# Kernel tuning notes

Hardware: AMD Instinct MI355X
Metric: run time of the kernel (lower is better)

Reference implementation:

```python
import jax, jax.numpy as jnp
import numpy as np

B = 131072
D_IN = 385          # 384-d embedding + 1 correctness feature
D_H = 192           # both trunk layers resolve to max(.,192)=192 per source
Q = 1000            # number of questions
C = 16              # classes per head (uniform padding of per-question heads)


def setup_inputs() -> dict:
    key = jax.random.key(0)
    ks = jax.random.split(key, 9)
    x = jax.random.normal(ks[0], (B, D_IN), dtype=jnp.float32)
    question_ids = jax.random.randint(ks[1], (B,), 0, Q, dtype=jnp.int32)
    is_correct = jax.random.randint(ks[2], (B,), 0, 2, dtype=jnp.int32)
    W1 = jax.random.normal(ks[3], (D_IN, D_H), dtype=jnp.float32) * 0.05
    b1 = jnp.zeros((D_H,), dtype=jnp.float32)
    W2 = jax.random.normal(ks[4], (D_H, D_H), dtype=jnp.float32) * 0.05
    b2 = jnp.zeros((D_H,), dtype=jnp.float32)
    # Head bank: slots [0,Q) = false heads, [Q,2Q) = true heads.
    W_heads = jax.random.normal(ks[5], (2 * Q, C, D_H), dtype=jnp.float32) * 0.05
    b_heads = jax.random.normal(ks[6], (2 * Q, C), dtype=jnp.float32) * 0.05
    return {"x": x, "question_ids": question_ids, "is_correct": is_correct,
            "W1": W1, "b1": b1, "W2": W2, "b2": b2,
            "W_heads": W_heads, "b_heads": b_heads}


def reference(x, question_ids, is_correct, W1, b1, W2, b2, W_heads, b_heads):
    # Shared trunk (eval mode: dropout = identity)
    h = jax.nn.relu(x @ W1 + b1)            # [B, 192]
    feat = jax.nn.relu(h @ W2 + b2)         # [B, 192]
    # Hard routing: pick true or false head for this question.
    Qn = W_heads.shape[0] // 2
    idx = question_ids + is_correct * Qn    # [B]
    Wq = W_heads[idx]                       # [B, C, 192] gather (memory-bound)
    bq = b_heads[idx]                       # [B, C]
    logits = jnp.einsum('bcd,bd->bc', Wq, feat) + bq  # per-sample routed linear
    return logits
```

## Files before the change

### kernel.cpp

```cpp
#include <hip/hip_runtime.h>
#include <hip/hip_bf16.h>
#include <stdint.h>
#include <stddef.h>


typedef short s8v __attribute__((ext_vector_type(8)));
typedef float f4v __attribute__((ext_vector_type(4)));
typedef float f4a __attribute__((ext_vector_type(4), aligned(4)));

typedef const void __attribute__((address_space(1))) *gas1_t;
typedef void __attribute__((address_space(3))) *las3_t;

namespace {
constexpr int kDin = 385;
constexpr int kDh  = 192;
constexpr int kQ   = 1000;
constexpr int kC   = 16;
constexpr int BM   = 64;
constexpr int BM2  = 128;
constexpr int NT   = 512;
constexpr int NK1  = 13;
constexpr int NK2  = 6;
constexpr int CHUNK = 12 * 64 * 8;
constexpr int H2   = 200;

constexpr size_t WS_W1   = 0;
constexpr size_t WS_W2   = 163840;
constexpr size_t WS_HIST = 245760;
constexpr size_t WS_CUR  = 253952;
constexpr size_t WS_PERM = 262144;

constexpr size_t WB_FEAT = 0;
constexpr size_t WB_W1   = 50331648;
constexpr size_t WB_W2   = WB_W1 + 159744;
constexpr size_t WB_HIST = WB_W2 + 73728;
constexpr size_t WB_CUR  = WB_HIST + 8192;
constexpr size_t WB_PERM = WB_CUR + 8192;
constexpr size_t WB_NEED = WB_PERM + 524288;
constexpr size_t WS_SANE_MAX = (1ull << 36);
}

__device__ __forceinline__ unsigned short f2bf(float f) {
  unsigned int u = __float_as_uint(f);
  u = u + 0x7fffu + ((u >> 16) & 1u);
  return (unsigned short)(u >> 16);
}

__device__ __forceinline__ unsigned int pk2(float lo, float hi) {
  union { __hip_bfloat162 h2; unsigned int u; } cv;
  cv.h2 = __float22bfloat162_rn(make_float2(lo, hi));
  return cv.u;
}

union s8u { s8v s; unsigned int u[4]; };

__device__ __forceinline__ void swz_one(const float* W, int K, int i,
                                        unsigned short* out) {
  int k = i / kDh;
  int c = i - k * kDh;
  float v = (k < K) ? W[(size_t)k * kDh + c] : 0.f;
  int oi = (k >> 5) * CHUNK + (((c >> 4) * 64 + ((k >> 3) & 3) * 16 + (c & 15)) << 3)
         + (k & 7);
  out[oi] = f2bf(v);
}

__global__ void combo_prep(const int* __restrict__ qid, const int* __restrict__ isc,
                           int B, int nbH,
                           const float* __restrict__ W1, const float* __restrict__ W2,
                           int* __restrict__ hist,
                           unsigned short* __restrict__ W1sw,
                           unsigned short* __restrict__ W2sw) {
  int bid = blockIdx.x;
  if (bid < nbH) {
    int i = bid * 256 + threadIdx.x;
    if (i < B) atomicAdd(&hist[qid[i] + isc[i] * kQ], 1);
  } else if (bid < nbH + 312) {
    swz_one(W1, kDin, (bid - nbH) * 256 + threadIdx.x, W1sw);
  } else {
    swz_one(W2, kDh, (bid - nbH - 312) * 256 + threadIdx.x, W2sw);
  }
}

__global__ __launch_bounds__(256)
void scatter2(const int* __restrict__ qid, const int* __restrict__ isc, int B,
              const int* __restrict__ hist, int* __restrict__ rank_ctr,
              int* __restrict__ perm) {
  __shared__ int sh[2048];
  __shared__ int ssum[256];
  int t = threadIdx.x;
  int4 a = ((const int4*)hist)[t * 2];
  int4 b = ((const int4*)hist)[t * 2 + 1];
  int s1 = a.x + a.y, s2 = s1 + a.z, s3 = s2 + a.w;
  int s4 = s3 + b.x, s5 = s4 + b.y, s6 = s5 + b.z, s7 = s6 + b.w;
  ssum[t] = s7;
  __syncthreads();
  #pragma unroll
  for (int d = 1; d < 256; d <<= 1) {
    int xv = (t >= d) ? ssum[t - d] : 0;
    __syncthreads();
    ssum[t] += xv;
    __syncthreads();
  }
  int base = ssum[t] - s7;
  sh[t * 8 + 0] = base;
  sh[t * 8 + 1] = base + a.x;
  sh[t * 8 + 2] = base + s1;
  sh[t * 8 + 3] = base + s2;
  sh[t * 8 + 4] = base + s3;
  sh[t * 8 + 5] = base + s4;
  sh[t * 8 + 6] = base + s5;
  sh[t * 8 + 7] = base + s6;
  __syncthreads();
  int i = blockIdx.x * 256 + t;
  if (i < B) {
    int h = qid[i] + isc[i] * kQ;
    int pos = sh[h] + atomicAdd(&rank_ctr[h], 1);
    perm[pos] = i;
  }
}

__device__ __forceinline__ void stage2(const unsigned short* gsrc,
                                       unsigned short* lbase, int tid) {
  const char* g = (const char*)gsrc + (size_t)tid * 16;
  char* l = (char*)lbase + ((tid >> 6) << 10);
  __builtin_amdgcn_global_load_lds((gas1_t)g, (las3_t)l, 16, 0, 0);
  if (tid < 256)
    __builtin_amdgcn_global_load_lds((gas1_t)(g + 8192), (las3_t)(l + 8192),
                                     16, 0, 0);
}

__global__ __launch_bounds__(NT, 4)
void trunk_k2(const float* __restrict__ x,
              const float* __restrict__ b1,
              const float* __restrict__ b2,
              const unsigned short* __restrict__ W1sw,
              const unsigned short* __restrict__ W2sw,
              unsigned short* __restrict__ featG) {
  __shared__ __align__(16) unsigned short hS[BM2 * H2];
  __shared__ __align__(16) unsigned short bS[2 * CHUNK];

  const int tid  = threadIdx.x;
  const int lane = tid & 63, wid = tid >> 6;
  const int m = lane & 15, quad = lane >> 4;
  const int w16 = wid * 16;
  const int row0 = blockIdx.x * BM2;

  const float* px = x + (size_t)(row0 + w16 + m) * kDin;

  stage2(W1sw, bS, tid);
  f4a c0 = *(const f4a*)(px + quad * 8);
  f4a c1 = *(const f4a*)(px + quad * 8 + 4);
  float tl = 0.f;

  f4v acc[12];
  #pragma unroll
  for (int t = 0; t < 12; ++t) acc[t] = (f4v){0.f, 0.f, 0.f, 0.f};
  __syncthreads();

  #pragma unroll
  for (int g = 0; g < NK1; ++g) {
    const unsigned short* np = (g < NK1 - 1)
        ? W1sw + (size_t)(g + 1) * CHUNK : W2sw;
    stage2(np, bS + ((g + 1) & 1) * CHUNK, tid);

    f4a n0, n1;
    if (g < NK1 - 2) {
      n0 = *(const f4a*)(px + (g + 1) * 32 + quad * 8);
      n1 = *(const f4a*)(px + (g + 1) * 32 + quad * 8 + 4);
    } else if (g == NK1 - 2) {
      tl = (quad == 0) ? px[384] : 0.f;
    }

    s8v a;
    if (g < NK1 - 1) {
      s8u ua;
      ua.u[0] = pk2(c0[0], c0[1]); ua.u[1] = pk2(c0[2], c0[3]);
      ua.u[2] = pk2(c1[0], c1[1]); ua.u[3] = pk2(c1[2], c1[3]);
      a = ua.s;
    } else {
      a = (s8v){0,0,0,0,0,0,0,0};
      a[0] = (short)f2bf(tl);
    }

    const unsigned short* bB = bS + (g & 1) * CHUNK;
    #pragma unroll
    for (int t = 0; t < 12; ++t) {
      s8v b = *(const s8v*)&bB[(t * 64 + lane) * 8];
      acc[t] = __builtin_amdgcn_mfma_f32_16x16x32_bf16(a, b, acc[t], 0, 0, 0);
    }

    if (g == NK1 - 1) {
      #pragma unroll
      for (int t = 0; t < 12; ++t) {
        int c = t * 16 + m;
        float bb = b1[c];
        #pragma unroll
        for (int r4 = 0; r4 < 4; ++r4) {
          int r = w16 + quad * 4 + r4;
          float v0 = acc[t][r4] + bb;
          hS[r * H2 + c] = f2bf(v0 > 0.f ? v0 : 0.f);
          acc[t][r4] = 0.f;
        }
      }
    }
    __syncthreads();
    if (g < NK1 - 2) { c0 = n0; c1 = n1; }
  }

  #pragma unroll
  for (int k2 = 0; k2 < NK2; ++k2) {
    const int g = NK1 + k2;
    if (k2 < NK2 - 1)
      stage2(W2sw + (size_t)(k2 + 1) * CHUNK,
             bS + ((g + 1) & 1) * CHUNK, tid);

    s8v a = *(const s8v*)&hS[(w16 + m) * H2 + k2 * 32 + quad * 8];
    const unsigned short* bB = bS + (g & 1) * CHUNK;
    #pragma unroll
    for (int t = 0; t < 12; ++t) {
      s8v b = *(const s8v*)&bB[(t * 64 + lane) * 8];
      acc[t] = __builtin_amdgcn_mfma_f32_16x16x32_bf16(a, b, acc[t], 0, 0, 0);
    }
    if (k2 < NK2 - 1) __syncthreads();
  }

  #pragma unroll
  for (int t = 0; t < 12; ++t) {
    int c = t * 16 + m;
    float bb = b2[c];
    #pragma unroll
    for (int r4 = 0; r4 < 4; ++r4) {
      int r = w16 + quad * 4 + r4;
      float v0 = acc[t][r4] + bb;
      hS[r * H2 + c] = f2bf(v0 > 0.f ? v0 : 0.f);
    }
  }
  __syncthreads();

  #pragma unroll
  for (int j = 0; j < 6; ++j) {
    int e = tid + j * NT;
    int row = e / 24, c8 = e - row * 24;
    *(s8v*)&featG[(size_t)(row0 + row) * kDh + c8 * 8] =
        *(const s8v*)&hS[row * H2 + c8 * 8];
  }
}

__global__ __launch_bounds__(NT, 8)
void head_k(const int* __restrict__ qid, const int* __restrict__ isc,
            const float* __restrict__ Wh, const float* __restrict__ bh,
            const unsigned short* __restrict__ featG,
            const int* __restrict__ perm, float* __restrict__ out) {
  __shared__ int permS[BM];
  __shared__ int idxS[BM];

  const int tid  = threadIdx.x;
  const int lane = tid & 63, wid = tid >> 6;
  const int m = lane & 15, quad = lane >> 4;
  const int rh = wid >> 1, ch = wid & 1;
  const int row0 = blockIdx.x * BM;

  if (tid < BM) {
    int p = perm[row0 + tid];
    permS[tid] = p;
    idxS[tid] = qid[p] + isc[p] * kQ;
  }
  __syncthreads();

  const int w16 = rh * 16;
  const unsigned short* fp = featG + (size_t)permS[w16 + m] * kDh + quad * 8;
  s8v f[6];
  #pragma unroll
  for (int kk = 0; kk < 6; ++kk) f[kk] = *(const s8v*)(fp + kk * 32);

  const int hm = idxS[w16 + m];
  const s8v zf = (s8v){0,0,0,0,0,0,0,0};
  unsigned rem = 0xFFFFu;
  int runIdx = 0;
  while (rem) {
    int r0 = (int)__builtin_ctz(rem);
    int h = idxS[w16 + r0];
    unsigned long long bal = __ballot(hm == h);
    unsigned mask16 = (unsigned)(bal & 0xFFFFu);
    rem &= ~mask16;
    if ((runIdx & 1) == ch) {
      bool valid = (hm == h);
      const float* wq = Wh + ((size_t)h * kC + m) * kDh + quad * 8;
      f4v acch = (f4v){0.f, 0.f, 0.f, 0.f};
      #pragma unroll
      for (int kk = 0; kk < 6; ++kk) {
        float4 wlo = *(const float4*)(wq + kk * 32);
        float4 whi = *(const float4*)(wq + kk * 32 + 4);
        s8u ub;
        ub.u[0] = pk2(wlo.x, wlo.y);
        ub.u[1] = pk2(wlo.z, wlo.w);
        ub.u[2] = pk2(whi.x, whi.y);
        ub.u[3] = pk2(whi.z, whi.w);
        s8v afr = valid ? f[kk] : zf;
        acch = __builtin_amdgcn_mfma_f32_16x16x32_bf16(afr, ub.s, acch, 0, 0, 0);
      }
      float bhv = bh[(size_t)h * kC + m];
      #pragma unroll
      for (int reg = 0; reg < 4; ++reg) {
        int r = quad * 4 + reg;
        if ((mask16 >> r) & 1u)
          out[(size_t)permS[w16 + r] * kC + m] = acch[reg] + bhv;
      }
    }
    runIdx++;
  }
}

__global__ __launch_bounds__(NT, 8)
void fused_qmlp8(const float* __restrict__ x,
                 const int*   __restrict__ qid,
                 const int*   __restrict__ isc,
                 const float* __restrict__ b1,
                 const float* __restrict__ b2,
                 const float* __restrict__ Wh,
                 const float* __restrict__ bh,
                 const unsigned short* __restrict__ W1sw,
                 const unsigned short* __restrict__ W2sw,
                 const int*   __restrict__ perm,
                 float* __restrict__ out) {
  __shared__ __align__(16) unsigned short hS[BM * H2];
  __shared__ __align__(16) unsigned short bS[CHUNK];
  __shared__ int permS[BM];
  __shared__ int idxS[BM];

  const int tid  = threadIdx.x;
  const int lane = tid & 63, wid = tid >> 6;
  const int m = lane & 15, quad = lane >> 4;
  const int rh = wid >> 1, ch = wid & 1;
  const int row0 = blockIdx.x * BM;

  {
    const char* g = (const char*)W1sw + (size_t)tid * 16;
    char* l = (char*)bS + ((tid >> 6) << 10);
    __builtin_amdgcn_global_load_lds((gas1_t)g, (las3_t)l, 16, 0, 0);
    if (tid < 256)
      __builtin_amdgcn_global_load_lds((gas1_t)(g + 8192), (las3_t)(l + 8192),
                                       16, 0, 0);
  }
  if (tid < BM) {
    int p = perm[row0 + tid];
    permS[tid] = p;
    idxS[tid] = qid[p] + isc[p] * kQ;
  }
  __syncthreads();

  const float* px = x + (size_t)permS[rh * 16 + m] * kDin;

  f4v acc[6];
  #pragma unroll
  for (int t = 0; t < 6; ++t) acc[t] = (f4v){0.f, 0.f, 0.f, 0.f};

  f4a c0 = *(const f4a*)(px + quad * 8);
  f4a c1 = *(const f4a*)(px + quad * 8 + 4);
  float tl = 0.f;

  #pragma unroll
  for (int kk = 0; kk < NK1; ++kk) {
    s8v a;
    if (kk < NK1 - 1) {
      s8u ua;
      ua.u[0] = pk2(c0[0], c0[1]); ua.u[1] = pk2(c0[2], c0[3]);
      ua.u[2] = pk2(c1[0], c1[1]); ua.u[3] = pk2(c1[2], c1[3]);
      a = ua.s;
    } else {
      a = (s8v){0,0,0,0,0,0,0,0};
      a[0] = (short)f2bf(tl);
    }

    #pragma unroll
    for (int t = 0; t < 6; ++t) {
      s8v b = *(const s8v*)&bS[((ch * 6 + t) * 64 + lane) * 8];
      acc[t] = __builtin_amdgcn_mfma_f32_16x16x32_bf16(a, b, acc[t], 0, 0, 0);
    }
    __syncthreads();

    {
      const unsigned short* np = (kk < NK1 - 1)
          ? W1sw + (size_t)(kk + 1) * CHUNK : W2sw;
      const char* g = (const char*)np + (size_t)tid * 16;
      char* l = (char*)bS + ((tid >> 6) << 10);
      __builtin_amdgcn_global_load_lds((gas1_t)g, (las3_t)l, 16, 0, 0);
      if (tid < 256)
        __builtin_amdgcn_global_load_lds((gas1_t)(g + 8192), (las3_t)(l + 8192),
                                         16, 0, 0);
    }
    if (kk < NK1 - 2) {
      c0 = *(const f4a*)(px + (kk + 1) * 32 + quad * 8);
      c1 = *(const f4a*)(px + (kk + 1) * 32 + quad * 8 + 4);
    } else if (kk == NK1 - 2) {
      tl = (quad == 0) ? px[384] : 0.f;
    }
    if (kk == NK1 - 1) {
      #pragma unroll
      for (int t = 0; t < 6; ++t) {
        int c = ch * 96 + t * 16 + m;
        float bb = b1[c];
        #pragma unroll
        for (int r4 = 0; r4 < 4; ++r4) {
          int r = rh * 16 + quad * 4 + r4;
          float v0 = acc[t][r4] + bb;
          hS[r * H2 + c] = f2bf(v0 > 0.f ? v0 : 0.f);
          acc[t][r4] = 0.f;
        }
      }
    }
    __syncthreads();
  }

  const int ar0 = (rh * 16 + m) * H2;
  #pragma unroll
  for (int k2 = 0; k2 < NK2; ++k2) {
    s8v a = *(const s8v*)&hS[ar0 + k2 * 32 + quad * 8];
    #pragma unroll
    for (int t = 0; t < 6; ++t) {
      s8v b = *(const s8v*)&bS[((ch * 6 + t) * 64 + lane) * 8];
      acc[t] = __builtin_amdgcn_mfma_f32_16x16x32_bf16(a, b, acc[t], 0, 0, 0);
    }
    __syncthreads();
    if (k2 < NK2 - 1) {
      const char* g = (const char*)(W2sw + (size_t)(k2 + 1) * CHUNK)
                    + (size_t)tid * 16;
      char* l = (char*)bS + ((tid >> 6) << 10);
      __builtin_amdgcn_global_load_lds((gas1_t)g, (las3_t)l, 16, 0, 0);
      if (tid < 256)
        __builtin_amdgcn_global_load_lds((gas1_t)(g + 8192), (las3_t)(l + 8192),
                                         16, 0, 0);
    } else {
      #pragma unroll
      for (int t = 0; t < 6; ++t) {
        int c = ch * 96 + t * 16 + m;
        float bb = b2[c];
        #pragma unroll
        for (int r4 = 0; r4 < 4; ++r4) {
          int r = rh * 16 + quad * 4 + r4;
          float v0 = acc[t][r4] + bb;
          hS[r * H2 + c] = f2bf(v0 > 0.f ? v0 : 0.f);
        }
      }
    }
    __syncthreads();
  }

  {
    const int w16 = rh * 16;
    const int hm = idxS[w16 + m];
    unsigned rem = 0xFFFFu;
    int runIdx = 0;
    while (rem) {
      int r0 = (int)__builtin_ctz(rem);
      int h = idxS[w16 + r0];
      unsigned long long bal = __ballot(hm == h);
      unsigned mask16 = (unsigned)(bal & 0xFFFFu);
      rem &= ~mask16;
      if ((runIdx & 1) == ch) {
        const float* wq = Wh + ((size_t)h * kC + m) * kDh + quad * 8;
        f4v acch = (f4v){0.f, 0.f, 0.f, 0.f};
        #pragma unroll
        for (int kk = 0; kk < 6; ++kk) {
          float4 wlo = *(const float4*)(wq + kk * 32);
          float4 whi = *(const float4*)(wq + kk * 32 + 4);
          s8u ub;
          ub.u[0] = pk2(wlo.x, wlo.y);
          ub.u[1] = pk2(wlo.z, wlo.w);
          ub.u[2] = pk2(whi.x, whi.y);
          ub.u[3] = pk2(whi.z, whi.w);
          s8v afr = *(const s8v*)&hS[(w16 + m) * H2 + kk * 32 + quad * 8];
          if (hm != h) afr = (s8v){0,0,0,0,0,0,0,0};
          acch = __builtin_amdgcn_mfma_f32_16x16x32_bf16(afr, ub.s, acch, 0, 0, 0);
        }
        float bhv = bh[(size_t)h * kC + m];
        #pragma unroll
        for (int reg = 0; reg < 4; ++reg) {
          int r = quad * 4 + reg;
          if ((mask16 >> r) & 1u)
            out[(size_t)permS[w16 + r] * kC + m] = acch[reg] + bhv;
        }
      }
      runIdx++;
    }
  }
}

extern "C" void kernel_launch(void* const* d_in, const int* in_sizes, int n_in,
                              void* d_out, int out_size, void* d_ws, size_t ws_size,
                              hipStream_t stream) {
  const float* x  = (const float*)d_in[0];
  const int*   qd = (const int*)  d_in[1];
  const int*   ic = (const int*)  d_in[2];
  const float* W1 = (const float*)d_in[3];
  const float* b1 = (const float*)d_in[4];
  const float* W2 = (const float*)d_in[5];
  const float* b2 = (const float*)d_in[6];
  const float* Wh = (const float*)d_in[7];
  const float* bh = (const float*)d_in[8];
  float* out = (float*)d_out;

  char* ws = (char*)d_ws;
  int B = in_sizes[1];
  int nbH = (B + 255) / 256;

  const bool big = (d_ws != nullptr) && (ws_size >= WB_NEED)
                 && (ws_size < WS_SANE_MAX);

  if (big) {
    unsigned short* featG = (unsigned short*)(ws + WB_FEAT);
    unsigned short* W1sw  = (unsigned short*)(ws + WB_W1);
    unsigned short* W2sw  = (unsigned short*)(ws + WB_W2);
    int* hist = (int*)(ws + WB_HIST);
    int* rank = (int*)(ws + WB_CUR);
    int* perm = (int*)(ws + WB_PERM);

    hipMemsetAsync(hist, 0, 4096 * sizeof(int), stream);
    combo_prep<<<nbH + 312 + 144, 256, 0, stream>>>(qd, ic, B, nbH, W1, W2,
                                                    hist, W1sw, W2sw);
    scatter2<<<(B + 255) / 256, 256, 0, stream>>>(qd, ic, B, hist, rank, perm);
    trunk_k2<<<B / BM2, NT, 0, stream>>>(x, b1, b2, W1sw, W2sw, featG);
    head_k<<<B / BM, NT, 0, stream>>>(qd, ic, Wh, bh, featG, perm, out);
  } else {
    unsigned short* W1sw = (unsigned short*)(ws + WS_W1);
    unsigned short* W2sw = (unsigned short*)(ws + WS_W2);
    int* hist = (int*)(ws + WS_HIST);
    int* rank = (int*)(ws + WS_CUR);
    int* perm = (int*)(ws + WS_PERM);

    hipMemsetAsync(hist, 0, 4096 * sizeof(int), stream);
    combo_prep<<<nbH + 312 + 144, 256, 0, stream>>>(qd, ic, B, nbH, W1, W2,
                                                    hist, W1sw, W2sw);
    scatter2<<<(B + 255) / 256, 256, 0, stream>>>(qd, ic, B, hist, rank, perm);
    fused_qmlp8<<<B / BM, NT, 0, stream>>>(x, qd, ic, b1, b2, Wh, bh,
                                           W1sw, W2sw, perm, out);
  }
}
```

Measured before the change: 400.2 us.

## Double trunk tile rows per block and stage x through LDS asynchronously

```diff
diff --git a/kernel.cpp b/kernel.cpp
--- a/kernel.cpp
+++ b/kernel.cpp
@@ -17,7 +17,7 @@
 constexpr int kQ   = 1000;
 constexpr int kC   = 16;
 constexpr int BM   = 64;
-constexpr int BM2  = 128;
+constexpr int BM2  = 256;
 constexpr int NT   = 512;
 constexpr int NK1  = 13;
 constexpr int NK2  = 6;
@@ -119,8 +119,8 @@
   }
 }
 
-__device__ __forceinline__ void stage2(const unsigned short* gsrc,
-                                       unsigned short* lbase, int tid) {
+__device__ __forceinline__ void stage_w(const unsigned short* gsrc,
+                                        unsigned short* lbase, int tid) {
   const char* g = (const char*)gsrc + (size_t)tid * 16;
   char* l = (char*)lbase + ((tid >> 6) << 10);
   __builtin_amdgcn_global_load_lds((gas1_t)g, (las3_t)l, 16, 0, 0);
@@ -129,8 +129,22 @@
                                      16, 0, 0);
 }
 
-__global__ __launch_bounds__(NT, 4)
-void trunk_k2(const float* __restrict__ x,
+__device__ __forceinline__ void stage_x(const float* xg, int row0, int g,
+                                        unsigned short* xbuf, int tid) {
+  #pragma unroll
+  for (int t = 0; t < 4; ++t) {
+    int s = tid + t * 512;
+    int r = s >> 3;
+    int j = s & 7;
+    const float* src = xg + (size_t)(row0 + r) * kDin + g * 32
+                     + ((j ^ (r & 7)) << 2);
+    char* l = (char*)xbuf + ((tid >> 6) << 10) + t * 8192;
+    __builtin_amdgcn_global_load_lds((gas1_t)src, (las3_t)l, 16, 0, 0);
+  }
+}
+
+__global__ __launch_bounds__(NT, 2)
+void trunk_k4(const float* __restrict__ x,
               const float* __restrict__ b1,
               const float* __restrict__ b2,
               const unsigned short* __restrict__ W1sw,
@@ -142,51 +156,67 @@
   const int tid  = threadIdx.x;
   const int lane = tid & 63, wid = tid >> 6;
   const int m = lane & 15, quad = lane >> 4;
-  const int w16 = wid * 16;
+  const int w32 = wid * 32;
   const int row0 = blockIdx.x * BM2;
-
-  const float* px = x + (size_t)(row0 + w16 + m) * kDin;
-
-  stage2(W1sw, bS, tid);
-  f4a c0 = *(const f4a*)(px + quad * 8);
-  f4a c1 = *(const f4a*)(px + quad * 8 + 4);
-  float tl = 0.f;
-
-  f4v acc[12];
-  #pragma unroll
-  for (int t = 0; t < 12; ++t) acc[t] = (f4v){0.f, 0.f, 0.f, 0.f};
+  const int z = m & 7;
+  const int u0 = (((quad << 1) ^ z) << 4);
+
+  stage_w(W1sw, bS, tid);
+  stage_x(x, row0, 0, (unsigned short*)hS, tid);
+
+  f4v accA[12], accB[12];
+  #pragma unroll
+  for (int t = 0; t < 12; ++t) {
+    accA[t] = (f4v){0.f, 0.f, 0.f, 0.f};
+    accB[t] = (f4v){0.f, 0.f, 0.f, 0.f};
+  }
+  float tl0 = 0.f, tl1 = 0.f;
   __syncthreads();
 
   #pragma unroll
   for (int g = 0; g < NK1; ++g) {
-    const unsigned short* np = (g < NK1 - 1)
-        ? W1sw + (size_t)(g + 1) * CHUNK : W2sw;
-    stage2(np, bS + ((g + 1) & 1) * CHUNK, tid);
-
-    f4a n0, n1;
-    if (g < NK1 - 2) {
-      n0 = *(const f4a*)(px + (g + 1) * 32 + quad * 8);
-      n1 = *(const f4a*)(px + (g + 1) * 32 + quad * 8 + 4);
-    } else if (g == NK1 - 2) {
-      tl = (quad == 0) ? px[384] : 0.f;
-    }
-
-    s8v a;
+    {
+      const unsigned short* np = (g < NK1 - 1)
+          ? W1sw + (size_t)(g + 1) * CHUNK : W2sw;
+      stage_w(np, bS + ((g + 1) & 1) * CHUNK, tid);
+    }
+    if (g < 11)
+      stage_x(x, row0, g + 1,
+              (unsigned short*)((char*)hS + ((g + 1) & 1) * 32768), tid);
+    if (g == 11) {
+      const float* px0 = x + (size_t)(row0 + w32 + m) * kDin;
+      tl0 = (quad == 0) ? px0[384] : 0.f;
+      tl1 = (quad == 0) ? px0[16 * kDin + 384] : 0.f;
+    }
+
+    s8v a0, a1;
     if (g < NK1 - 1) {
-      s8u ua;
+      const char* xb = (const char*)hS + (g & 1) * 32768;
+      const char* rb0 = xb + (w32 + m) * 128;
+      f4a c0 = *(const f4a*)(rb0 + u0);
+      f4a c1 = *(const f4a*)(rb0 + (u0 ^ 16));
+      const char* rb1 = rb0 + 2048;
+      f4a c2 = *(const f4a*)(rb1 + u0);
+      f4a c3 = *(const f4a*)(rb1 + (u0 ^ 16));
+      s8u ua, ub;
       ua.u[0] = pk2(c0[0], c0[1]); ua.u[1] = pk2(c0[2], c0[3]);
       ua.u[2] = pk2(c1[0], c1[1]); ua.u[3] = pk2(c1[2], c1[3]);
-      a = ua.s;
+      ub.u[0] = pk2(c2[0], c2[1]); ub.u[1] = pk2(c2[2], c2[3]);
+      ub.u[2] = pk2(c3[0], c3[1]); ub.u[3] = pk2(c3[2], c3[3]);
+      a0 = ua.s; a1 = ub.s;
     } else {
-      a = (s8v){0,0,0,0,0,0,0,0};
-      a[0] = (short)f2bf(tl);
+      a0 = (s8v){0,0,0,0,0,0,0,0};
+      a1 = (s8v){0,0,0,0,0,0,0,0};
+      a0[0] = (short)f2bf(tl0);
+      a1[0] = (short)f2bf(tl1);
     }
 
     const unsigned short* bB = bS + (g & 1) * CHUNK;
     #pragma unroll
     for (int t = 0; t < 12; ++t) {
       s8v b = *(const s8v*)&bB[(t * 64 + lane) * 8];
-      acc[t] = __builtin_amdgcn_mfma_f32_16x16x32_bf16(a, b, acc[t], 0, 0, 0);
+      accA[t] = __builtin_amdgcn_mfma_f32_16x16x32_bf16(a0, b, accA[t], 0, 0, 0);
+      accB[t] = __builtin_amdgcn_mfma_f32_16x16x32_bf16(a1, b, accB[t], 0, 0, 0);
     }
 
     if (g == NK1 - 1) {
@@ -196,30 +226,33 @@
         float bb = b1[c];
         #pragma unroll
         for (int r4 = 0; r4 < 4; ++r4) {
-          int r = w16 + quad * 4 + r4;
-          float v0 = acc[t][r4] + bb;
-          hS[r * H2 + c] = f2bf(v0 > 0.f ? v0 : 0.f);
-          acc[t][r4] = 0.f;
+          float v0 = accA[t][r4] + bb;
+          hS[(w32 + quad * 4 + r4) * H2 + c] = f2bf(v0 > 0.f ? v0 : 0.f);
+          float v1 = accB[t][r4] + bb;
+          hS[(w32 + 16 + quad * 4 + r4) * H2 + c] = f2bf(v1 > 0.f ? v1 : 0.f);
+          accA[t][r4] = 0.f;
+          accB[t][r4] = 0.f;
         }
       }
     }
     __syncthreads();
-    if (g < NK1 - 2) { c0 = n0; c1 = n1; }
   }
 
   #pragma unroll
   for (int k2 = 0; k2 < NK2; ++k2) {
     const int g = NK1 + k2;
     if (k2 < NK2 - 1)
-      stage2(W2sw + (size_t)(k2 + 1) * CHUNK,
-             bS + ((g + 1) & 1) * CHUNK, tid);
-
-    s8v a = *(const s8v*)&hS[(w16 + m) * H2 + k2 * 32 + quad * 8];
+      stage_w(W2sw + (size_t)(k2 + 1) * CHUNK,
+              bS + ((g + 1) & 1) * CHUNK, tid);
+
+    s8v a0 = *(const s8v*)&hS[(w32 + m) * H2 + k2 * 32 + quad * 8];
+    s8v a1 = *(const s8v*)&hS[(w32 + 16 + m) * H2 + k2 * 32 + quad * 8];
     const unsigned short* bB = bS + (g & 1) * CHUNK;
     #pragma unroll
     for (int t = 0; t < 12; ++t) {
       s8v b = *(const s8v*)&bB[(t * 64 + lane) * 8];
-      acc[t] = __builtin_amdgcn_mfma_f32_16x16x32_bf16(a, b, acc[t], 0, 0, 0);
+      accA[t] = __builtin_amdgcn_mfma_f32_16x16x32_bf16(a0, b, accA[t], 0, 0, 0);
+      accB[t] = __builtin_amdgcn_mfma_f32_16x16x32_bf16(a1, b, accB[t], 0, 0, 0);
     }
     if (k2 < NK2 - 1) __syncthreads();
   }
@@ -230,17 +263,18 @@
     float bb = b2[c];
     #pragma unroll
     for (int r4 = 0; r4 < 4; ++r4) {
-      int r = w16 + quad * 4 + r4;
-      float v0 = acc[t][r4] + bb;
-      hS[r * H2 + c] = f2bf(v0 > 0.f ? v0 : 0.f);
+      float v0 = accA[t][r4] + bb;
+      hS[(w32 + quad * 4 + r4) * H2 + c] = f2bf(v0 > 0.f ? v0 : 0.f);
+      float v1 = accB[t][r4] + bb;
+      hS[(w32 + 16 + quad * 4 + r4) * H2 + c] = f2bf(v1 > 0.f ? v1 : 0.f);
     }
   }
   __syncthreads();
 
   #pragma unroll
-  for (int j = 0; j < 6; ++j) {
-    int e = tid + j * NT;
-    int row = e / 24, c8 = e - row * 24;
+  for (int j = 0; j < 12; ++j) {
+    int e = lane + j * 64;
+    int row = w32 + e / 24, c8 = e - (e / 24) * 24;
     *(s8v*)&featG[(size_t)(row0 + row) * kDh + c8 * 8] =
         *(const s8v*)&hS[row * H2 + c8 * 8];
   }
@@ -519,7 +553,7 @@
     combo_prep<<<nbH + 312 + 144, 256, 0, stream>>>(qd, ic, B, nbH, W1, W2,
                                                     hist, W1sw, W2sw);
     scatter2<<<(B + 255) / 256, 256, 0, stream>>>(qd, ic, B, hist, rank, perm);
-    trunk_k2<<<B / BM2, NT, 0, stream>>>(x, b1, b2, W1sw, W2sw, featG);
+    trunk_k4<<<B / BM2, NT, 0, stream>>>(x, b1, b2, W1sw, W2sw, featG);
     head_k<<<B / BM, NT, 0, stream>>>(qd, ic, Wh, bh, featG, perm, out);
   } else {
     unsigned short* W1sw = (unsigned short*)(ws + WS_W1);
```

Result: no change. 406.4 us (+1.5%).
